# Optimization experiments

Hardware: AMD Instinct MI355X
Metric: run time of the kernel (lower is better)

## Reference

```python
import jax, jax.numpy as jnp
import numpy as np

R = 8  # patch radius (init kwarg)


def setup_inputs() -> dict:
    key = jax.random.key(0)
    k1, k2, k3 = jax.random.split(key, 3)
    B, H, W, N = 8, 1024, 1024, 4096
    image1 = jax.random.normal(k1, (B, 1, H, W), dtype=jnp.float32)
    image2 = jax.random.normal(k2, (B, 1, H, W), dtype=jnp.float32)
    # (x1, y1, x2, y2) integer pixel coords in [0, H-1]
    matches = jax.random.randint(k3, (B, N, 4), 0, H, dtype=jnp.int32)
    return {"image1": image1, "image2": image2, "matches": matches}


def _normalize(p):
    # per-patch zero-mean / unit-std (unbiased std, matching torch.std)
    m = p.mean(axis=-1, keepdims=True)
    s = p.std(axis=-1, keepdims=True, ddof=1)
    return (p - m) / (s + 1e-4)


def reference(image1, image2, matches):
    r = R
    d = 2 * r + 1
    # offset grid, flattened row-major: lines[i,j]=i, columns[i,j]=j
    lines = jnp.repeat(jnp.arange(d, dtype=jnp.int32), d)   # [d^2]
    cols = jnp.tile(jnp.arange(d, dtype=jnp.int32), d)      # [d^2]
    # original M = [lines, columns, lines, columns]
    off = jnp.stack([lines, cols, lines, cols], axis=0)      # [4, d^2]
    idx = matches[..., None].astype(jnp.int32) + off          # [B, N, 4, d^2]

    def pad(im):  # [B,1,H,W] -> [B, H+2r, W+2r]
        return jnp.pad(im[:, 0], ((0, 0), (r, r), (r, r)))

    img1p, img2p = pad(image1), pad(image2)
    b = jnp.arange(matches.shape[0])[:, None, None]           # [B,1,1]
    # rows come from y-coord columns (1,3), cols from x-coord columns (0,2)
    p1 = img1p[b, idx[:, :, 1, :], idx[:, :, 0, :]]           # [B, N, d^2]
    p2 = img2p[b, idx[:, :, 3, :], idx[:, :, 2, :]]           # [B, N, d^2]
    return jnp.concatenate([_normalize(p1), _normalize(p2)], axis=-1)  # [B, N, 2*d^2]
```

## Files before the change

kernel.cpp:

```cpp
#include <hip/hip_runtime.h>
#include <hip/hip_bf16.h>


#define IMG_H 1024
#define IMG_W 1024
#define NMATCH 4096
#define DPATCH 17
#define NPATCH 289
#define RAD 8

__global__ __launch_bounds__(256) void extract_patch_kernel(
    const float* __restrict__ img1,
    const float* __restrict__ img2,
    const int* __restrict__ matches,
    float* __restrict__ out)
{
    const int tid  = blockIdx.x * blockDim.x + threadIdx.x;
    const int wave = tid >> 6;
    const int lane = tid & 63;
    const int pair  = wave >> 1;
    const int which = wave & 1;

    const int* m = matches + pair * 4;
    const int mx = m[which ? 2 : 0];
    const int my = m[which ? 3 : 1];

    const int b = pair >> 12;
    const float* __restrict__ imgb =
        (which ? img2 : img1) + (size_t)b * (IMG_H * IMG_W);

    float v[5];
    float sum = 0.f, sumsq = 0.f;
#pragma unroll
    for (int k = 0; k < 5; ++k) {
        const int j = lane + (k << 6);
        float val = 0.f;
        if (j < NPATCH) {
            const int iy = my + (j % DPATCH) - RAD;
            const int ix = mx + (j / DPATCH) - RAD;
            if ((unsigned)iy < IMG_H && (unsigned)ix < IMG_W) {
                val = imgb[iy * IMG_W + ix];
            }
        }
        v[k] = val;
        sum   += val;
        sumsq += val * val;
    }

#pragma unroll
    for (int off = 32; off > 0; off >>= 1) {
        sum   += __shfl_xor(sum,   off, 64);
        sumsq += __shfl_xor(sumsq, off, 64);
    }

    const float mean = sum * (1.0f / 289.0f);
    float var = (sumsq - 289.0f * mean * mean) * (1.0f / 288.0f);
    var = fmaxf(var, 0.0f);
    const float inv = 1.0f / (sqrtf(var) + 1e-4f);

    float* __restrict__ o = out + (size_t)pair * 578 + which * NPATCH;
#pragma unroll
    for (int k = 0; k < 5; ++k) {
        const int j = lane + (k << 6);
        if (j < NPATCH) {
            o[j] = (v[k] - mean) * inv;
        }
    }
}

extern "C" void kernel_launch(void* const* d_in, const int* in_sizes, int n_in,
                              void* d_out, int out_size, void* d_ws, size_t ws_size,
                              hipStream_t stream) {
    const float* img1  = (const float*)d_in[0];
    const float* img2  = (const float*)d_in[1];
    const int* matches = (const int*)d_in[2];
    float* out         = (float*)d_out;

    const int n_waves = 8 * NMATCH * 2;
    dim3 block(256);
    dim3 grid(n_waves * 64 / 256);
    hipLaunchKernelGGL(extract_patch_kernel, grid, block, 0, stream,
                       img1, img2, matches, out);
}
```

Measured before the change: 152.1 us.

## Bucket patch tasks by spatial tile and extract from shared-memory image tiles

Adds a counting-sort pipeline (histogram, scan, scatter) that groups the 65536 patch tasks into 48x48 spatial buckets per image. Each bucket block then loads a 64x64 padded tile into LDS with float4 loads and extracts all its patches from shared memory, so overlapping patches no longer gather scattered pixels from global memory repeatedly. Output stores become nontemporal. The trade-off is four extra small kernel launches, atomics on the histogram, and a single-block scan that runs serially. Buckets also vary in size, so some blocks may carry uneven work.

```diff
diff --git a/kernel.cpp b/kernel.cpp
--- a/kernel.cpp
+++ b/kernel.cpp
@@ -4,66 +4,178 @@
 
 #define IMG_H 1024
 #define IMG_W 1024
-#define NMATCH 4096
 #define DPATCH 17
 #define NPATCH 289
 #define RAD 8
+#define HW (IMG_H * IMG_W)
+#define NTASK 65536
+#define BKT 48
+#define TILE 64
+#define GB 22
+#define NBUCKET (16 * GB * GB)
+#define TSTRIDE 65
+
+
+__device__ __forceinline__ int task_key(const int* __restrict__ matches, int t) {
+    const int pair  = t >> 1;
+    const int which = t & 1;
+    const int mx = matches[pair * 4 + (which ? 2 : 0)];
+    const int my = matches[pair * 4 + (which ? 3 : 1)];
+    const int b  = pair >> 12;
+    return (((b * 2 + which) * GB) + my / BKT) * GB + mx / BKT;
+}
+
+__global__ __launch_bounds__(256) void zero_hist_kernel(int* __restrict__ hist) {
+    for (int i = threadIdx.x; i < NBUCKET; i += 256) hist[i] = 0;
+}
+
+__global__ __launch_bounds__(256) void hist_kernel(
+    const int* __restrict__ matches, int* __restrict__ hist) {
+    const int t = blockIdx.x * blockDim.x + threadIdx.x;
+    atomicAdd(&hist[task_key(matches, t)], 1);
+}
+
+__global__ __launch_bounds__(256) void scan_kernel(
+    int* __restrict__ hist, int* __restrict__ starts) {
+    __shared__ int wsum[4];
+    const int t = threadIdx.x;
+    const int lane = t & 63, w = t >> 6;
+    const int per = 32;
+    const int base = t * per;
+    int s = 0;
+    for (int i = 0; i < per; ++i) {
+        const int idx = base + i;
+        if (idx < NBUCKET) s += hist[idx];
+    }
+    int pre = s;
+#pragma unroll
+    for (int off = 1; off < 64; off <<= 1) {
+        const int x = __shfl_up(pre, off, 64);
+        if (lane >= off) pre += x;
+    }
+    if (lane == 63) wsum[w] = pre;
+    __syncthreads();
+    int wbase = 0;
+#pragma unroll
+    for (int k = 0; k < 4; ++k) if (k < w) wbase += wsum[k];
+    int run = wbase + pre - s;
+    for (int i = 0; i < per; ++i) {
+        const int idx = base + i;
+        if (idx < NBUCKET) {
+            const int c = hist[idx];
+            hist[idx] = run;
+            starts[idx] = run;
+            run += c;
+        }
+    }
+    if (t == 255) starts[NBUCKET] = run;
+}
+
+__global__ __launch_bounds__(256) void scatter_kernel(
+    const int* __restrict__ matches, int* __restrict__ hist,
+    int* __restrict__ tasks) {
+    const int t = blockIdx.x * blockDim.x + threadIdx.x;
+    const int pos = atomicAdd(&hist[task_key(matches, t)], 1);
+    tasks[pos] = t;
+}
 
 __global__ __launch_bounds__(256) void extract_patch_kernel(
     const float* __restrict__ img1,
     const float* __restrict__ img2,
     const int* __restrict__ matches,
+    const int* __restrict__ starts,
+    const int* __restrict__ tasks,
     float* __restrict__ out)
 {
-    const int tid  = blockIdx.x * blockDim.x + threadIdx.x;
-    const int wave = tid >> 6;
-    const int lane = tid & 63;
-    const int pair  = wave >> 1;
-    const int which = wave & 1;
-
-    const int* m = matches + pair * 4;
-    const int mx = m[which ? 2 : 0];
-    const int my = m[which ? 3 : 1];
-
-    const int b = pair >> 12;
-    const float* __restrict__ imgb =
-        (which ? img2 : img1) + (size_t)b * (IMG_H * IMG_W);
-
-    float v[5];
-    float sum = 0.f, sumsq = 0.f;
+    __shared__ float tile[TILE * TSTRIDE];
+
+    const int bid = blockIdx.x;
+    const int start = starts[bid];
+    const int end   = starts[bid + 1];
+    if (start == end) return;
+
+    const int bx = bid % GB;
+    const int tmp = bid / GB;
+    const int by = tmp % GB;
+    const int iw = tmp / GB;
+    const int which = iw & 1;
+    const int b = iw >> 1;
+    const float* __restrict__ imgb = (which ? img2 : img1) + (size_t)b * HW;
+
+    const int oy = by * BKT - RAD;
+    const int ox = bx * BKT - RAD;
+
+    for (int u = threadIdx.x; u < TILE * 16; u += 256) {
+        const int tr = u >> 4;
+        const int tc = (u & 15) * 4;
+        const int gy = oy + tr;
+        const int gx = ox + tc;
+        float4 val = make_float4(0.f, 0.f, 0.f, 0.f);
+        if ((unsigned)gy < IMG_H) {
+            const float* __restrict__ rowp = imgb + gy * IMG_W;
+            if ((unsigned)gx <= (unsigned)(IMG_W - 4)) {
+                val = *(const float4*)(rowp + gx);
+            } else {
+                float* vv = (float*)&val;
+#pragma unroll
+                for (int cc = 0; cc < 4; ++cc) {
+                    const int x = gx + cc;
+                    if ((unsigned)x < IMG_W) vv[cc] = rowp[x];
+                }
+            }
+        }
+        const int la = tr * TSTRIDE + tc;
+        tile[la + 0] = val.x; tile[la + 1] = val.y;
+        tile[la + 2] = val.z; tile[la + 3] = val.w;
+    }
+    __syncthreads();
+
+    const int lane  = threadIdx.x & 63;
+    const int wslot = threadIdx.x >> 6;
+
+    int ofs[5];
 #pragma unroll
     for (int k = 0; k < 5; ++k) {
         const int j = lane + (k << 6);
-        float val = 0.f;
-        if (j < NPATCH) {
-            const int iy = my + (j % DPATCH) - RAD;
-            const int ix = mx + (j / DPATCH) - RAD;
-            if ((unsigned)iy < IMG_H && (unsigned)ix < IMG_W) {
-                val = imgb[iy * IMG_W + ix];
+        ofs[k] = (j % DPATCH) * TSTRIDE + (j / DPATCH);
+    }
+
+    for (int i = start + wslot; i < end; i += 4) {
+        const int t = tasks[i];
+        const int pair = t >> 1;
+        const int wh = t & 1;
+        const int mx = matches[pair * 4 + (wh ? 2 : 0)];
+        const int my = matches[pair * 4 + (wh ? 3 : 1)];
+        const int pbase = (my - by * BKT) * TSTRIDE + (mx - bx * BKT);
+
+        float v[5];
+        float s = 0.f, q = 0.f;
+#pragma unroll
+        for (int k = 0; k < 5; ++k) {
+            const int j = lane + (k << 6);
+            float x = 0.f;
+            if (j < NPATCH) x = tile[pbase + ofs[k]];
+            v[k] = x;
+            s += x;
+            q += x * x;
+        }
+#pragma unroll
+        for (int off = 32; off > 0; off >>= 1) {
+            s += __shfl_xor(s, off, 64);
+            q += __shfl_xor(q, off, 64);
+        }
+        const float mean = s * (1.0f / 289.0f);
+        float var = (q - 289.0f * mean * mean) * (1.0f / 288.0f);
+        var = fmaxf(var, 0.0f);
+        const float inv = 1.0f / (sqrtf(var) + 1e-4f);
+
+        float* __restrict__ o = out + (size_t)pair * 578 + wh * NPATCH;
+#pragma unroll
+        for (int k = 0; k < 5; ++k) {
+            const int j = lane + (k << 6);
+            if (j < NPATCH) {
+                __builtin_nontemporal_store((v[k] - mean) * inv, &o[j]);
             }
-        }
-        v[k] = val;
-        sum   += val;
-        sumsq += val * val;
-    }
-
-#pragma unroll
-    for (int off = 32; off > 0; off >>= 1) {
-        sum   += __shfl_xor(sum,   off, 64);
-        sumsq += __shfl_xor(sumsq, off, 64);
-    }
-
-    const float mean = sum * (1.0f / 289.0f);
-    float var = (sumsq - 289.0f * mean * mean) * (1.0f / 288.0f);
-    var = fmaxf(var, 0.0f);
-    const float inv = 1.0f / (sqrtf(var) + 1e-4f);
-
-    float* __restrict__ o = out + (size_t)pair * 578 + which * NPATCH;
-#pragma unroll
-    for (int k = 0; k < 5; ++k) {
-        const int j = lane + (k << 6);
-        if (j < NPATCH) {
-            o[j] = (v[k] - mean) * inv;
         }
     }
 }
@@ -76,9 +188,17 @@
     const int* matches = (const int*)d_in[2];
     float* out         = (float*)d_out;
 
-    const int n_waves = 8 * NMATCH * 2;
-    dim3 block(256);
-    dim3 grid(n_waves * 64 / 256);
-    hipLaunchKernelGGL(extract_patch_kernel, grid, block, 0, stream,
-                       img1, img2, matches, out);
-}
+    int* w = (int*)d_ws;
+    int* hist   = w;
+    int* starts = w + 8192;
+    int* tasks  = w + 16384;
+
+    hipLaunchKernelGGL(zero_hist_kernel, dim3(1), dim3(256), 0, stream, hist);
+    hipLaunchKernelGGL(hist_kernel, dim3(NTASK / 256), dim3(256), 0, stream,
+                       matches, hist);
+    hipLaunchKernelGGL(scan_kernel, dim3(1), dim3(256), 0, stream, hist, starts);
+    hipLaunchKernelGGL(scatter_kernel, dim3(NTASK / 256), dim3(256), 0, stream,
+                       matches, hist, tasks);
+    hipLaunchKernelGGL(extract_patch_kernel, dim3(NBUCKET), dim3(256), 0, stream,
+                       img1, img2, matches, starts, tasks, out);
+}
```

Result: slower. 171.0 us (+12.4%).
